# Performance work log

Measured on AMD Instinct MI355X. Metric: run time of the kernel, lower is better.

## Reference

```python
import jax, jax.numpy as jnp
import numpy as np

D = 2048      # in_features (model dim)
H = 1408      # d_intermediate (hidden per expert)
E = 16        # n_routed_experts
T = 16384     # flattened tokens
K = 4         # top_k experts per token


def setup_inputs() -> dict:
    key = jax.random.key(0)
    k1, k2, k3, k4, k5 = jax.random.split(key, 5)
    x = jax.random.normal(k1, (T, D), dtype=jnp.float32)
    weights = jax.random.uniform(k2, (T, K), dtype=jnp.float32)
    indices = jax.random.randint(k3, (T, K), 0, E)
    # Stacked GatedMLP params (bias=False as in mamba's GatedMLP):
    # fc1: [2H, D] per expert, fc2: [D, H] per expert
    W1 = jax.random.normal(k4, (E, 2 * H, D), dtype=jnp.float32) * (D ** -0.5)
    W2 = jax.random.normal(k5, (E, D, H), dtype=jnp.float32) * (H ** -0.5)
    return {"x": x, "weights": weights, "indices": indices, "W1": W1, "W2": W2}


def reference(x, weights, indices, W1, W2):
    # y[t] = sum_i ( GatedMLP_i(x[t]) * sum_k weights[t,k] * [indices[t,k]==i] )
    n_experts = W1.shape[0]
    y = jnp.zeros_like(x)
    for i in range(n_experts):  # small fixed expert loop
        # combined routing weight of expert i per token (handles duplicate hits like += in torch)
        cw = jnp.sum(weights * (indices == i), axis=-1)      # [T]
        h = x @ W1[i].T                                      # [T, 2H]
        u, g = jnp.split(h, 2, axis=-1)                      # chunk(2, dim=-1): (y, gate)
        out = (u * jax.nn.silu(g)) @ W2[i].T                 # [T, D]
        y = y + out * cw[:, None]
    return y
```

## Files before the change

### kernel.cpp

```cpp
#include <hip/hip_runtime.h>

#define D_ 2048
#define H_ 1408
#define E_ 16
#define T_ 16384
#define K_ 4
#define TK_ 65536
#define BM_ 256
#define BK_ 64
#define MAXT_ 272

typedef __attribute__((ext_vector_type(8))) short bf16x8;
typedef __attribute__((ext_vector_type(4))) float f32x4;
typedef __attribute__((ext_vector_type(4))) unsigned short u16x4;
typedef __attribute__((ext_vector_type(8))) unsigned short u16x8;

#define M_COUNTS 0
#define M_OFF    16
#define M_CUR    33
#define M_NT     49
#define M_TE     64
#define M_TR     (64 + MAXT_)
#define M_TN     (64 + 2*MAXT_)

#define XB_OFF   0ULL
#define W1B_OFF  67108864ULL
#define W2B_OFF  (W1B_OFF + 188743680ULL)
#define ACT_OFF  (W2B_OFF + 94371840ULL)
#define PERM_OFF (ACT_OFF + 184549376ULL)
#define WGT_OFF  (PERM_OFF + 262144ULL)
#define META_B   (WGT_OFF + 262144ULL)
#define INV_OFF  (META_B + 65536ULL)
#define YP_OFF   (INV_OFF + 262144ULL)
#define WS_NEED  (YP_OFF + 268435456ULL)

#define SBAR()  __builtin_amdgcn_s_barrier()
#define SCHED() __builtin_amdgcn_sched_barrier(0)
#define LGK0()  asm volatile("s_waitcnt lgkmcnt(0)" ::: "memory")
#define LGK2()  asm volatile("s_waitcnt lgkmcnt(2)" ::: "memory")
#define LGK4()  asm volatile("s_waitcnt lgkmcnt(4)" ::: "memory")
#define LGK6()  asm volatile("s_waitcnt lgkmcnt(6)" ::: "memory")
#define VM6()   asm volatile("s_waitcnt vmcnt(6)" ::: "memory")
#define PRIO1() __builtin_amdgcn_s_setprio(1)
#define PRIO0() __builtin_amdgcn_s_setprio(0)

static __device__ __forceinline__ unsigned short f2bf(float f) {
  unsigned u = __builtin_bit_cast(unsigned, f);
  u += 0x7fffu + ((u >> 16) & 1u);
  return (unsigned short)(u >> 16);
}
static __device__ __forceinline__ float bf2f(unsigned short s) {
  return __builtin_bit_cast(float, (unsigned)s << 16);
}

static __device__ __forceinline__ void gload16(const void* g, unsigned ldsOff) {
  __builtin_amdgcn_global_load_lds(
      (const __attribute__((address_space(1))) unsigned int*)(unsigned long long)g,
      (__attribute__((address_space(3))) unsigned int*)(unsigned long long)ldsOff,
      16, 0, 0);
}

__global__ void cvt3_kernel(const float* __restrict__ x, const float* __restrict__ W1,
                            const float* __restrict__ W2, unsigned short* __restrict__ xb,
                            unsigned short* __restrict__ w1b, unsigned short* __restrict__ w2b) {
  const long long base = ((long long)blockIdx.x * blockDim.x + threadIdx.x) * 4;
  const long long stride = (long long)gridDim.x * blockDim.x * 4;
  for (long long i = base; i < (long long)T_ * D_; i += stride) {
    float4 v = *reinterpret_cast<const float4*>(x + i);
    u16x4 o = { f2bf(v.x), f2bf(v.y), f2bf(v.z), f2bf(v.w) };
    *reinterpret_cast<u16x4*>(xb + i) = o;
  }
  for (long long i = base; i < (long long)E_ * 2 * H_ * D_; i += stride) {
    float4 v = *reinterpret_cast<const float4*>(W1 + i);
    u16x4 o = { f2bf(v.x), f2bf(v.y), f2bf(v.z), f2bf(v.w) };
    *reinterpret_cast<u16x4*>(w1b + i) = o;
  }
  for (long long i = base; i < (long long)E_ * D_ * H_; i += stride) {
    float4 v = *reinterpret_cast<const float4*>(W2 + i);
    u16x4 o = { f2bf(v.x), f2bf(v.y), f2bf(v.z), f2bf(v.w) };
    *reinterpret_cast<u16x4*>(w2b + i) = o;
  }
}

__global__ void route_count(const int* __restrict__ idx, int* __restrict__ meta) {
  int i = blockIdx.x * 256 + threadIdx.x;
  if (i < TK_) atomicAdd(&meta[M_COUNTS + idx[i]], 1);
}

__global__ void scan_build(int* __restrict__ meta) {
  if (threadIdx.x != 0 || blockIdx.x != 0) return;
  int off = 0;
  for (int e = 0; e < E_; ++e) {
    meta[M_OFF + e] = off;
    meta[M_CUR + e] = off;
    off += meta[M_COUNTS + e];
  }
  meta[M_OFF + E_] = off;
  int nt = 0;
  for (int e = 0; e < E_; ++e) {
    int c = meta[M_COUNTS + e], b = meta[M_OFF + e];
    for (int r = 0; r < c; r += BM_) {
      meta[M_TE + nt] = e;
      meta[M_TR + nt] = b + r;
      meta[M_TN + nt] = (c - r < BM_) ? (c - r) : BM_;
      ++nt;
    }
  }
  meta[M_NT] = nt;
}

__global__ void route_fill(const int* __restrict__ idx, const float* __restrict__ wts,
                           int* __restrict__ meta, int* __restrict__ perm,
                           float* __restrict__ wgt, int* __restrict__ inv) {
  int i = blockIdx.x * 256 + threadIdx.x;
  if (i >= TK_) return;
  int e = idx[i];
  int pos = atomicAdd(&meta[M_CUR + e], 1);
  perm[pos] = i >> 2;
  wgt[pos] = wts[i];
  inv[i] = pos;
}

__global__ __launch_bounds__(512, 2) void gemm1_kernel(
    const char* __restrict__ xb, const char* __restrict__ w1b,
    const int* __restrict__ perm, const int* __restrict__ meta,
    unsigned short* __restrict__ act) {
  __shared__ char lds[131072];
  int bid = (int)blockIdx.x;
  bid = (bid & 7) * (int)(gridDim.x >> 3) + (bid >> 3);
  const int tb = bid / 11;
  const int cb = bid - tb * 11;
  if (tb >= meta[M_NT]) return;
  const int e = meta[M_TE + tb];
  const int row0 = meta[M_TR + tb];
  const int nrows = meta[M_TN + tb];
  const int tid = threadIdx.x, lane = tid & 63, wid = tid >> 6;
  const int wr = wid >> 2, wc = wid & 3;
  const unsigned ldsBase = (unsigned)(unsigned long long)&lds[0];
  constexpr int NT = D_ / BK_;

  const char* aSrc[4];
  const char* bSrc[4];
  {
    const int r8 = tid >> 3;
    const unsigned colb0 = (unsigned)(tid & 7) * 16u;
#pragma unroll
    for (int i = 0; i < 4; ++i) {
      const int r = r8 + i * 64;
      const unsigned colb = colb0 ^ ((unsigned)(r & 7) << 4);
      const int rc = (r < nrows) ? r : 0;
      aSrc[i] = xb + (size_t)perm[row0 + rc] * 4096 + colb;
      const int w1row = (i < 2) ? (cb * 128 + r) : (H_ + cb * 128 + (r - 128));
      bSrc[i] = w1b + (size_t)e * (2 * H_) * 4096ULL + (size_t)w1row * 4096 + colb;
    }
  }

  const int l15 = lane & 15, hi = lane >> 4;
  const unsigned swz = (unsigned)(l15 & 7) << 4;
  unsigned aOff[8], bOffU[2], bOffG[2];
#pragma unroll
  for (int m = 0; m < 8; ++m) {
    const int row = wr * 128 + m * 16 + l15;
    aOff[m] = (unsigned)(row * 128) + (((unsigned)hi * 16u) ^ swz);
  }
#pragma unroll
  for (int n = 0; n < 2; ++n) {
    const int ru = wc * 32 + n * 16 + l15;
    bOffU[n] = 65536u + (unsigned)(ru * 128) + (((unsigned)hi * 16u) ^ swz);
    const int rg = ru + 128;
    bOffG[n] = 65536u + (unsigned)(rg * 128) + (((unsigned)hi * 16u) ^ swz);
  }

  f32x4 aU[8][2], aG[8][2];
#pragma unroll
  for (int m = 0; m < 8; ++m)
#pragma unroll
    for (int n = 0; n < 2; ++n) {
      aU[m][n] = (f32x4){0.f, 0.f, 0.f, 0.f};
      aG[m][n] = (f32x4){0.f, 0.f, 0.f, 0.f};
    }

  auto STAGE_A = [&](int t, int h) {
    const int tt = (t < NT) ? t : (NT - 1);
    const size_t kb = (size_t)tt * 128;
    const unsigned dst = ldsBase + (unsigned)(t & 1) * 32768u + (unsigned)h * 16384u + (unsigned)tid * 16u;
    gload16(aSrc[h * 2 + 0] + kb, dst);
    gload16(aSrc[h * 2 + 1] + kb, dst + 8192u);
  };
  auto STAGE_B = [&](int t, int h) {
    const int tt = (t < NT) ? t : (NT - 1);
    const size_t kb = (size_t)tt * 128;
    const unsigned dst = ldsBase + 65536u + (unsigned)(t & 1) * 32768u + (unsigned)h * 16384u + (unsigned)tid * 16u;
    gload16(bSrc[h * 2 + 0] + kb, dst);
    gload16(bSrc[h * 2 + 1] + kb, dst + 8192u);
  };

  STAGE_B(0, 0); STAGE_B(0, 1); STAGE_A(0, 0); STAGE_A(0, 1);
  STAGE_B(1, 0); STAGE_B(1, 1); STAGE_A(1, 0);
  VM6(); SCHED(); SBAR();

  for (int t = 0; t < NT; ++t) {
    const char* base = lds + (unsigned)(t & 1) * 32768u;
    bf16x8 aLo[4][2], aHi[4][2], bu[2][2], bg[2][2];

#pragma unroll
    for (int ks = 0; ks < 2; ++ks) {
#pragma unroll
      for (int m = 0; m < 4; ++m)
        aLo[m][ks] = *reinterpret_cast<const bf16x8*>(base + (aOff[m] ^ (unsigned)(ks << 6)));
#pragma unroll
      for (int n = 0; n < 2; ++n)
        bu[n][ks] = *reinterpret_cast<const bf16x8*>(base + (bOffU[n] ^ (unsigned)(ks << 6)));
    }
    STAGE_A(t + 1, 1);
    SCHED(); SBAR(); LGK6(); SCHED();
    PRIO1();
#pragma unroll
    for (int m = 0; m < 4; ++m)
#pragma unroll
      for (int n = 0; n < 2; ++n)
        aU[m][n] = __builtin_amdgcn_mfma_f32_16x16x32_bf16(aLo[m][0], bu[n][0], aU[m][n], 0, 0, 0);
    LGK0(); SCHED();
#pragma unroll
    for (int m = 0; m < 4; ++m)
#pragma unroll
      for (int n = 0; n < 2; ++n)
        aU[m][n] = __builtin_amdgcn_mfma_f32_16x16x32_bf16(aLo[m][1], bu[n][1], aU[m][n], 0, 0, 0);
    PRIO0(); SCHED(); SBAR();

#pragma unroll
    for (int ks = 0; ks < 2; ++ks)
#pragma unroll
      for (int n = 0; n < 2; ++n)
        bg[n][ks] = *reinterpret_cast<const bf16x8*>(base + (bOffG[n] ^ (unsigned)(ks << 6)));
    STAGE_B(t + 2, 0);
    SCHED(); SBAR(); LGK2(); SCHED();
    PRIO1();
#pragma unroll
    for (int m = 0; m < 4; ++m)
#pragma unroll
      for (int n = 0; n < 2; ++n)
        aG[m][n] = __builtin_amdgcn_mfma_f32_16x16x32_bf16(aLo[m][0], bg[n][0], aG[m][n], 0, 0, 0);
    LGK0(); SCHED();
#pragma unroll
    for (int m = 0; m < 4; ++m)
#pragma unroll
      for (int n = 0; n < 2; ++n)
        aG[m][n] = __builtin_amdgcn_mfma_f32_16x16x32_bf16(aLo[m][1], bg[n][1], aG[m][n], 0, 0, 0);
    PRIO0(); SCHED(); SBAR();

#pragma unroll
    for (int ks = 0; ks < 2; ++ks)
#pragma unroll
      for (int m = 0; m < 4; ++m)
        aHi[m][ks] = *reinterpret_cast<const bf16x8*>(base + (aOff[4 + m] ^ (unsigned)(ks << 6)));
    STAGE_B(t + 2, 1);
    SCHED(); SBAR(); LGK4(); SCHED();
    PRIO1();
#pragma unroll
    for (int m = 0; m < 4; ++m)
#pragma unroll
      for (int n = 0; n < 2; ++n)
        aU[4 + m][n] = __builtin_amdgcn_mfma_f32_16x16x32_bf16(aHi[m][0], bu[n][0], aU[4 + m][n], 0, 0, 0);
    LGK0(); SCHED();
#pragma unroll
    for (int m = 0; m < 4; ++m)
#pragma unroll
      for (int n = 0; n < 2; ++n)
        aU[4 + m][n] = __builtin_amdgcn_mfma_f32_16x16x32_bf16(aHi[m][1], bu[n][1], aU[4 + m][n], 0, 0, 0);
    PRIO0(); SCHED(); SBAR();

    STAGE_A(t + 2, 0);
    VM6(); SCHED(); SBAR();
    PRIO1();
#pragma unroll
    for (int ks = 0; ks < 2; ++ks)
#pragma unroll
      for (int m = 0; m < 4; ++m)
#pragma unroll
        for (int n = 0; n < 2; ++n)
          aG[4 + m][n] = __builtin_amdgcn_mfma_f32_16x16x32_bf16(aHi[m][ks], bg[n][ks], aG[4 + m][n], 0, 0, 0);
    PRIO0(); SCHED(); SBAR();
  }

#pragma unroll
  for (int m = 0; m < 8; ++m)
#pragma unroll
    for (int j = 0; j < 4; ++j) {
      const int r = wr * 128 + m * 16 + hi * 4 + j;
      if (r < nrows) {
        const size_t rowBase = (size_t)(row0 + r) * H_ + (size_t)cb * 128 + (size_t)wc * 32;
#pragma unroll
        for (int n = 0; n < 2; ++n) {
          const float u = aU[m][n][j];
          const float g = aG[m][n][j];
          act[rowBase + n * 16 + l15] = f2bf(u * (g / (1.0f + __expf(-g))));
        }
      }
    }
}

template <int ATOMIC>
__global__ __launch_bounds__(512, 2) void gemm2_kernel(
    const char* __restrict__ actb, const char* __restrict__ w2b,
    const int* __restrict__ perm, const float* __restrict__ wgt,
    const int* __restrict__ meta, unsigned short* __restrict__ yp,
    float* __restrict__ y) {
  __shared__ char lds[131072];
  int bid = (int)blockIdx.x;
  bid = (bid & 7) * (int)(gridDim.x >> 3) + (bid >> 3);
  const int tb = bid >> 3;
  const int cb = bid & 7;
  if (tb >= meta[M_NT]) return;
  const int e = meta[M_TE + tb];
  const int row0 = meta[M_TR + tb];
  const int nrows = meta[M_TN + tb];
  const int tid = threadIdx.x, lane = tid & 63, wid = tid >> 6;
  const int wr = wid >> 2, wc = wid & 3;
  const unsigned ldsBase = (unsigned)(unsigned long long)&lds[0];
  constexpr int NT = H_ / BK_;

  const char* aSrc[4];
  const char* bSrc[4];
  {
    const int r8 = tid >> 3;
    const unsigned colb0 = (unsigned)(tid & 7) * 16u;
#pragma unroll
    for (int i = 0; i < 4; ++i) {
      const int r = r8 + i * 64;
      const unsigned colb = colb0 ^ ((unsigned)(r & 7) << 4);
      const int rc = (r < nrows) ? r : 0;
      aSrc[i] = actb + (size_t)(row0 + rc) * (H_ * 2) + colb;
      const int brow = cb * 256 + r;
      bSrc[i] = w2b + (size_t)e * D_ * (H_ * 2) + (size_t)brow * (H_ * 2) + colb;
    }
  }

  const int l15 = lane & 15, hi = lane >> 4;
  const unsigned swz = (unsigned)(l15 & 7) << 4;
  unsigned aOff[8], bOff[4];
#pragma unroll
  for (int m = 0; m < 8; ++m) {
    const int row = wr * 128 + m * 16 + l15;
    aOff[m] = (unsigned)(row * 128) + (((unsigned)hi * 16u) ^ swz);
  }
#pragma unroll
  for (int n = 0; n < 4; ++n) {
    const int rb = wc * 64 + n * 16 + l15;
    bOff[n] = 65536u + (unsigned)(rb * 128) + (((unsigned)hi * 16u) ^ swz);
  }

  f32x4 acc[8][4];
#pragma unroll
  for (int m = 0; m < 8; ++m)
#pragma unroll
    for (int n = 0; n < 4; ++n) acc[m][n] = (f32x4){0.f, 0.f, 0.f, 0.f};

  auto STAGE_A = [&](int t, int h) {
    const int tt = (t < NT) ? t : (NT - 1);
    const size_t kb = (size_t)tt * 128;
    const unsigned dst = ldsBase + (unsigned)(t & 1) * 32768u + (unsigned)h * 16384u + (unsigned)tid * 16u;
    gload16(aSrc[h * 2 + 0] + kb, dst);
    gload16(aSrc[h * 2 + 1] + kb, dst + 8192u);
  };
  auto STAGE_B = [&](int t, int h) {
    const int tt = (t < NT) ? t : (NT - 1);
    const size_t kb = (size_t)tt * 128;
    const unsigned dst = ldsBase + 65536u + (unsigned)(t & 1) * 32768u + (unsigned)h * 16384u + (unsigned)tid * 16u;
    gload16(bSrc[h * 2 + 0] + kb, dst);
    gload16(bSrc[h * 2 + 1] + kb, dst + 8192u);
  };

  STAGE_B(0, 0); STAGE_B(0, 1); STAGE_A(0, 0); STAGE_A(0, 1);
  STAGE_B(1, 0); STAGE_B(1, 1); STAGE_A(1, 0);
  VM6(); SCHED(); SBAR();

  for (int t = 0; t < NT; ++t) {
    const char* base = lds + (unsigned)(t & 1) * 32768u;
    bf16x8 aLo[4][2], aHi[4][2], b[4][2];

#pragma unroll
    for (int ks = 0; ks < 2; ++ks) {
#pragma unroll
      for (int m = 0; m < 4; ++m)
        aLo[m][ks] = *reinterpret_cast<const bf16x8*>(base + (aOff[m] ^ (unsigned)(ks << 6)));
#pragma unroll
      for (int n = 0; n < 2; ++n)
        b[n][ks] = *reinterpret_cast<const bf16x8*>(base + (bOff[n] ^ (unsigned)(ks << 6)));
    }
    STAGE_A(t + 1, 1);
    SCHED(); SBAR(); LGK6(); SCHED();
    PRIO1();
#pragma unroll
    for (int m = 0; m < 4; ++m)
#pragma unroll
      for (int n = 0; n < 2; ++n)
        acc[m][n] = __builtin_amdgcn_mfma_f32_16x16x32_bf16(aLo[m][0], b[n][0], acc[m][n], 0, 0, 0);
    LGK0(); SCHED();
#pragma unroll
    for (int m = 0; m < 4; ++m)
#pragma unroll
      for (int n = 0; n < 2; ++n)
        acc[m][n] = __builtin_amdgcn_mfma_f32_16x16x32_bf16(aLo[m][1], b[n][1], acc[m][n], 0, 0, 0);
    PRIO0(); SCHED(); SBAR();

#pragma unroll
    for (int ks = 0; ks < 2; ++ks)
#pragma unroll
      for (int n = 2; n < 4; ++n)
        b[n][ks] = *reinterpret_cast<const bf16x8*>(base + (bOff[n] ^ (unsigned)(ks << 6)));
    STAGE_B(t + 2, 0);
    SCHED(); SBAR(); LGK2(); SCHED();
    PRIO1();
#pragma unroll
    for (int m = 0; m < 4; ++m)
#pragma unroll
      for (int n = 2; n < 4; ++n)
        acc[m][n] = __builtin_amdgcn_mfma_f32_16x16x32_bf16(aLo[m][0], b[n][0], acc[m][n], 0, 0, 0);
    LGK0(); SCHED();
#pragma unroll
    for (int m = 0; m < 4; ++m)
#pragma unroll
      for (int n = 2; n < 4; ++n)
        acc[m][n] = __builtin_amdgcn_mfma_f32_16x16x32_bf16(aLo[m][1], b[n][1], acc[m][n], 0, 0, 0);
    PRIO0(); SCHED(); SBAR();

#pragma unroll
    for (int ks = 0; ks < 2; ++ks)
#pragma unroll
      for (int m = 0; m < 4; ++m)
        aHi[m][ks] = *reinterpret_cast<const bf16x8*>(base + (aOff[4 + m] ^ (unsigned)(ks << 6)));
    STAGE_B(t + 2, 1);
    SCHED(); SBAR(); LGK4(); SCHED();
    PRIO1();
#pragma unroll
    for (int m = 0; m < 4; ++m)
#pragma unroll
      for (int n = 0; n < 2; ++n)
        acc[4 + m][n] = __builtin_amdgcn_mfma_f32_16x16x32_bf16(aHi[m][0], b[n][0], acc[4 + m][n], 0, 0, 0);
    LGK0(); SCHED();
#pragma unroll
    for (int m = 0; m < 4; ++m)
#pragma unroll
      for (int n = 0; n < 2; ++n)
        acc[4 + m][n] = __builtin_amdgcn_mfma_f32_16x16x32_bf16(aHi[m][1], b[n][1], acc[4 + m][n], 0, 0, 0);
    PRIO0(); SCHED(); SBAR();

    STAGE_A(t + 2, 0);
    VM6(); SCHED(); SBAR();
    PRIO1();
#pragma unroll
    for (int ks = 0; ks < 2; ++ks)
#pragma unroll
      for (int m = 0; m < 4; ++m)
#pragma unroll
        for (int n = 2; n < 4; ++n)
          acc[4 + m][n] = __builtin_amdgcn_mfma_f32_16x16x32_bf16(aHi[m][ks], b[n][ks], acc[4 + m][n], 0, 0, 0);
    PRIO0(); SCHED(); SBAR();
  }

#pragma unroll
  for (int m = 0; m < 8; ++m)
#pragma unroll
    for (int j = 0; j < 4; ++j) {
      const int r = wr * 128 + m * 16 + hi * 4 + j;
      if (r < nrows) {
        const float w = wgt[row0 + r];
        if (ATOMIC) {
          const int token = perm[row0 + r];
          float* yrow = y + (size_t)token * D_ + (size_t)cb * 256 + (size_t)wc * 64;
#pragma unroll
          for (int n = 0; n < 4; ++n)
            unsafeAtomicAdd(&yrow[n * 16 + l15], acc[m][n][j] * w);
        } else {
          unsigned short* prow = yp + (size_t)(row0 + r) * D_ + (size_t)cb * 256 + (size_t)wc * 64;
#pragma unroll
          for (int n = 0; n < 4; ++n)
            prow[n * 16 + l15] = f2bf(acc[m][n][j] * w);
        }
      }
    }
}

__global__ __launch_bounds__(256) void gather_kernel(
    const unsigned short* __restrict__ yp, const int* __restrict__ inv,
    float* __restrict__ y) {
  const int t = blockIdx.x;
  const int d0 = threadIdx.x * 8;
  int pos[4];
#pragma unroll
  for (int k = 0; k < 4; ++k) pos[k] = inv[t * 4 + k];
  float s[8];
#pragma unroll
  for (int i = 0; i < 8; ++i) s[i] = 0.f;
#pragma unroll
  for (int k = 0; k < 4; ++k) {
    u16x8 v = *reinterpret_cast<const u16x8*>(yp + (size_t)pos[k] * D_ + d0);
#pragma unroll
    for (int i = 0; i < 8; ++i) s[i] += bf2f(v[i]);
  }
  float4 lo = {s[0], s[1], s[2], s[3]}, hi4 = {s[4], s[5], s[6], s[7]};
  *reinterpret_cast<float4*>(y + (size_t)t * D_ + d0) = lo;
  *reinterpret_cast<float4*>(y + (size_t)t * D_ + d0 + 4) = hi4;
}

extern "C" void kernel_launch(void* const* d_in, const int* in_sizes, int n_in,
                              void* d_out, int out_size, void* d_ws, size_t ws_size,
                              hipStream_t stream) {
  const float* x   = (const float*)d_in[0];
  const float* wts = (const float*)d_in[1];
  const int*   idx = (const int*)d_in[2];
  const float* W1  = (const float*)d_in[3];
  const float* W2  = (const float*)d_in[4];
  float* y = (float*)d_out;
  char* ws = (char*)d_ws;

  unsigned short* xb  = (unsigned short*)(ws + XB_OFF);
  unsigned short* w1b = (unsigned short*)(ws + W1B_OFF);
  unsigned short* w2b = (unsigned short*)(ws + W2B_OFF);
  unsigned short* act = (unsigned short*)(ws + ACT_OFF);
  int*   perm = (int*)(ws + PERM_OFF);
  float* wgt  = (float*)(ws + WGT_OFF);
  int*   meta = (int*)(ws + META_B);
  int*   inv  = (int*)(ws + INV_OFF);
  unsigned short* yp = (unsigned short*)(ws + YP_OFF);

  const bool useYp = (ws_size >= (size_t)WS_NEED);

  hipMemsetAsync(meta, 0, 64 * sizeof(int), stream);
  if (!useYp) hipMemsetAsync(d_out, 0, (size_t)out_size * sizeof(float), stream);

  cvt3_kernel<<<4096, 256, 0, stream>>>(x, W1, W2, xb, w1b, w2b);

  route_count<<<TK_ / 256, 256, 0, stream>>>(idx, meta);
  scan_build<<<1, 64, 0, stream>>>(meta);
  route_fill<<<TK_ / 256, 256, 0, stream>>>(idx, wts, meta, perm, wgt, inv);

  gemm1_kernel<<<MAXT_ * (H_ / 128), 512, 0, stream>>>(
      (const char*)xb, (const char*)w1b, perm, meta, act);

  if (useYp) {
    gemm2_kernel<0><<<MAXT_ * (D_ / 256), 512, 0, stream>>>(
        (const char*)act, (const char*)w2b, perm, wgt, meta, yp, y);
    gather_kernel<<<T_, 256, 0, stream>>>(yp, inv, y);
  } else {
    gemm2_kernel<1><<<MAXT_ * (D_ / 256), 512, 0, stream>>>(
        (const char*)act, (const char*)w2b, perm, wgt, meta, yp, y);
  }
}
```

Before: 1.722 ms.

## Use hybrid bf16 partial buffer plus atomic tail to fit smaller workspace

Reorganizes the workspace so the partial-output buffer aliases the dead xb/w1b region. This lets the non-atomic bf16 partial path run without the large extra workspace. Rows below a fixed position threshold write bf16 partials that are gathered later, and the remaining rows use atomic adds into a zeroed output. The gather kernel now does a read-modify-write on y, and the output must always be memset. This avoids falling back to all-atomic accumulation when workspace is limited, at the cost of an extra memset and the y read in the gather.

```diff
diff --git a/kernel.cpp b/kernel.cpp
--- a/kernel.cpp
+++ b/kernel.cpp
@@ -9,6 +9,7 @@
 #define BM_ 256
 #define BK_ 64
 #define MAXT_ 272
+#define P1_ 61440
 
 typedef __attribute__((ext_vector_type(8))) short bf16x8;
 typedef __attribute__((ext_vector_type(4))) float f32x4;
@@ -23,16 +24,15 @@
 #define M_TR     (64 + MAXT_)
 #define M_TN     (64 + 2*MAXT_)
 
-#define XB_OFF   0ULL
-#define W1B_OFF  67108864ULL
-#define W2B_OFF  (W1B_OFF + 188743680ULL)
-#define ACT_OFF  (W2B_OFF + 94371840ULL)
-#define PERM_OFF (ACT_OFF + 184549376ULL)
+#define META_B   0ULL
+#define PERM_OFF 65536ULL
 #define WGT_OFF  (PERM_OFF + 262144ULL)
-#define META_B   (WGT_OFF + 262144ULL)
-#define INV_OFF  (META_B + 65536ULL)
-#define YP_OFF   (INV_OFF + 262144ULL)
-#define WS_NEED  (YP_OFF + 268435456ULL)
+#define INV_OFF  (WGT_OFF + 262144ULL)
+#define ACT_OFF  1048576ULL
+#define W2B_OFF  (ACT_OFF + 184549376ULL)
+#define XB_OFF   (W2B_OFF + 92274688ULL)
+#define W1B_OFF  (XB_OFF + 67108864ULL)
+#define YP_OFF   XB_OFF
 
 #define SBAR()  __builtin_amdgcn_s_barrier()
 #define SCHED() __builtin_amdgcn_sched_barrier(0)
@@ -300,7 +300,6 @@
     }
 }
 
-template <int ATOMIC>
 __global__ __launch_bounds__(512, 2) void gemm2_kernel(
     const char* __restrict__ actb, const char* __restrict__ w2b,
     const int* __restrict__ perm, const float* __restrict__ wgt,
@@ -465,18 +464,19 @@
     for (int j = 0; j < 4; ++j) {
       const int r = wr * 128 + m * 16 + hi * 4 + j;
       if (r < nrows) {
-        const float w = wgt[row0 + r];
-        if (ATOMIC) {
-          const int token = perm[row0 + r];
+        const int posr = row0 + r;
+        const float w = wgt[posr];
+        if (posr < P1_) {
+          unsigned short* prow = yp + (size_t)posr * D_ + (size_t)cb * 256 + (size_t)wc * 64;
+#pragma unroll
+          for (int n = 0; n < 4; ++n)
+            prow[n * 16 + l15] = f2bf(acc[m][n][j] * w);
+        } else {
+          const int token = perm[posr];
           float* yrow = y + (size_t)token * D_ + (size_t)cb * 256 + (size_t)wc * 64;
 #pragma unroll
           for (int n = 0; n < 4; ++n)
             unsafeAtomicAdd(&yrow[n * 16 + l15], acc[m][n][j] * w);
-        } else {
-          unsigned short* prow = yp + (size_t)(row0 + r) * D_ + (size_t)cb * 256 + (size_t)wc * 64;
-#pragma unroll
-          for (int n = 0; n < 4; ++n)
-            prow[n * 16 + l15] = f2bf(acc[m][n][j] * w);
         }
       }
     }
@@ -495,13 +495,19 @@
   for (int i = 0; i < 8; ++i) s[i] = 0.f;
 #pragma unroll
   for (int k = 0; k < 4; ++k) {
-    u16x8 v = *reinterpret_cast<const u16x8*>(yp + (size_t)pos[k] * D_ + d0);
-#pragma unroll
-    for (int i = 0; i < 8; ++i) s[i] += bf2f(v[i]);
-  }
-  float4 lo = {s[0], s[1], s[2], s[3]}, hi4 = {s[4], s[5], s[6], s[7]};
-  *reinterpret_cast<float4*>(y + (size_t)t * D_ + d0) = lo;
-  *reinterpret_cast<float4*>(y + (size_t)t * D_ + d0 + 4) = hi4;
+    if (pos[k] < P1_) {
+      u16x8 v = *reinterpret_cast<const u16x8*>(yp + (size_t)pos[k] * D_ + d0);
+#pragma unroll
+      for (int i = 0; i < 8; ++i) s[i] += bf2f(v[i]);
+    }
+  }
+  float* yrow = y + (size_t)t * D_ + d0;
+  float4 lo = *reinterpret_cast<const float4*>(yrow);
+  float4 hi4 = *reinterpret_cast<const float4*>(yrow + 4);
+  lo.x += s[0]; lo.y += s[1]; lo.z += s[2]; lo.w += s[3];
+  hi4.x += s[4]; hi4.y += s[5]; hi4.z += s[6]; hi4.w += s[7];
+  *reinterpret_cast<float4*>(yrow) = lo;
+  *reinterpret_cast<float4*>(yrow + 4) = hi4;
 }
 
 extern "C" void kernel_launch(void* const* d_in, const int* in_sizes, int n_in,
@@ -515,20 +521,18 @@
   float* y = (float*)d_out;
   char* ws = (char*)d_ws;
 
+  int*   meta = (int*)(ws + META_B);
+  int*   perm = (int*)(ws + PERM_OFF);
+  float* wgt  = (float*)(ws + WGT_OFF);
+  int*   inv  = (int*)(ws + INV_OFF);
+  unsigned short* act = (unsigned short*)(ws + ACT_OFF);
+  unsigned short* w2b = (unsigned short*)(ws + W2B_OFF);
   unsigned short* xb  = (unsigned short*)(ws + XB_OFF);
   unsigned short* w1b = (unsigned short*)(ws + W1B_OFF);
-  unsigned short* w2b = (unsigned short*)(ws + W2B_OFF);
-  unsigned short* act = (unsigned short*)(ws + ACT_OFF);
-  int*   perm = (int*)(ws + PERM_OFF);
-  float* wgt  = (float*)(ws + WGT_OFF);
-  int*   meta = (int*)(ws + META_B);
-  int*   inv  = (int*)(ws + INV_OFF);
-  unsigned short* yp = (unsigned short*)(ws + YP_OFF);
-
-  const bool useYp = (ws_size >= (size_t)WS_NEED);
+  unsigned short* yp  = (unsigned short*)(ws + YP_OFF);
 
   hipMemsetAsync(meta, 0, 64 * sizeof(int), stream);
-  if (!useYp) hipMemsetAsync(d_out, 0, (size_t)out_size * sizeof(float), stream);
+  hipMemsetAsync(d_out, 0, (size_t)out_size * sizeof(float), stream);
 
   cvt3_kernel<<<4096, 256, 0, stream>>>(x, W1, W2, xb, w1b, w2b);
 
@@ -539,12 +543,8 @@
   gemm1_kernel<<<MAXT_ * (H_ / 128), 512, 0, stream>>>(
       (const char*)xb, (const char*)w1b, perm, meta, act);
 
-  if (useYp) {
-    gemm2_kernel<0><<<MAXT_ * (D_ / 256), 512, 0, stream>>>(
-        (const char*)act, (const char*)w2b, perm, wgt, meta, yp, y);
-    gather_kernel<<<T_, 256, 0, stream>>>(yp, inv, y);
-  } else {
-    gemm2_kernel<1><<<MAXT_ * (D_ / 256), 512, 0, stream>>>(
-        (const char*)act, (const char*)w2b, perm, wgt, meta, yp, y);
-  }
-}
+  gemm2_kernel<<<MAXT_ * (D_ / 256), 512, 0, stream>>>(
+      (const char*)act, (const char*)w2b, perm, wgt, meta, yp, y);
+
+  gather_kernel<<<T_, 256, 0, stream>>>(yp, inv, y);
+}
```

New measurement: 1.800 ms. 1.05x slower.

## Drop workgroup barriers in GEMM main loops and scatter output via atomics

Applied to the files above, without the earlier changes.

Removes several s_barrier calls inside the main loops of both GEMM kernels, keeping only the per-wave LDS waitcnt and the one barrier after the vmcnt wait. Drops the bf16 per-slot partial buffer and its gather kernel. The second GEMM now always accumulates weighted results straight into the zeroed fp32 output with atomic adds. The aim is to cut cross-wave stalls, one kernel launch and the partial-buffer traffic, in exchange for float atomic contention and a possible LDS reuse race.

```diff
diff --git a/kernel.cpp b/kernel.cpp
--- a/kernel.cpp
+++ b/kernel.cpp
@@ -13,7 +13,6 @@
 typedef __attribute__((ext_vector_type(8))) short bf16x8;
 typedef __attribute__((ext_vector_type(4))) float f32x4;
 typedef __attribute__((ext_vector_type(4))) unsigned short u16x4;
-typedef __attribute__((ext_vector_type(8))) unsigned short u16x8;
 
 #define M_COUNTS 0
 #define M_OFF    16
@@ -30,9 +29,6 @@
 #define PERM_OFF (ACT_OFF + 184549376ULL)
 #define WGT_OFF  (PERM_OFF + 262144ULL)
 #define META_B   (WGT_OFF + 262144ULL)
-#define INV_OFF  (META_B + 65536ULL)
-#define YP_OFF   (INV_OFF + 262144ULL)
-#define WS_NEED  (YP_OFF + 268435456ULL)
 
 #define SBAR()  __builtin_amdgcn_s_barrier()
 #define SCHED() __builtin_amdgcn_sched_barrier(0)
@@ -49,9 +45,6 @@
   u += 0x7fffu + ((u >> 16) & 1u);
   return (unsigned short)(u >> 16);
 }
-static __device__ __forceinline__ float bf2f(unsigned short s) {
-  return __builtin_bit_cast(float, (unsigned)s << 16);
-}
 
 static __device__ __forceinline__ void gload16(const void* g, unsigned ldsOff) {
   __builtin_amdgcn_global_load_lds(
@@ -111,14 +104,13 @@
 
 __global__ void route_fill(const int* __restrict__ idx, const float* __restrict__ wts,
                            int* __restrict__ meta, int* __restrict__ perm,
-                           float* __restrict__ wgt, int* __restrict__ inv) {
+                           float* __restrict__ wgt) {
   int i = blockIdx.x * 256 + threadIdx.x;
   if (i >= TK_) return;
   int e = idx[i];
   int pos = atomicAdd(&meta[M_CUR + e], 1);
   perm[pos] = i >> 2;
   wgt[pos] = wts[i];
-  inv[i] = pos;
 }
 
 __global__ __launch_bounds__(512, 2) void gemm1_kernel(
@@ -213,7 +205,7 @@
         bu[n][ks] = *reinterpret_cast<const bf16x8*>(base + (bOffU[n] ^ (unsigned)(ks << 6)));
     }
     STAGE_A(t + 1, 1);
-    SCHED(); SBAR(); LGK6(); SCHED();
+    LGK6(); SCHED();
     PRIO1();
 #pragma unroll
     for (int m = 0; m < 4; ++m)
@@ -234,7 +226,7 @@
       for (int n = 0; n < 2; ++n)
         bg[n][ks] = *reinterpret_cast<const bf16x8*>(base + (bOffG[n] ^ (unsigned)(ks << 6)));
     STAGE_B(t + 2, 0);
-    SCHED(); SBAR(); LGK2(); SCHED();
+    LGK2(); SCHED();
     PRIO1();
 #pragma unroll
     for (int m = 0; m < 4; ++m)
@@ -255,7 +247,7 @@
       for (int m = 0; m < 4; ++m)
         aHi[m][ks] = *reinterpret_cast<const bf16x8*>(base + (aOff[4 + m] ^ (unsigned)(ks << 6)));
     STAGE_B(t + 2, 1);
-    SCHED(); SBAR(); LGK4(); SCHED();
+    LGK4(); SCHED();
     PRIO1();
 #pragma unroll
     for (int m = 0; m < 4; ++m)
@@ -280,7 +272,7 @@
 #pragma unroll
         for (int n = 0; n < 2; ++n)
           aG[4 + m][n] = __builtin_amdgcn_mfma_f32_16x16x32_bf16(aHi[m][ks], bg[n][ks], aG[4 + m][n], 0, 0, 0);
-    PRIO0(); SCHED(); SBAR();
+    PRIO0(); SCHED();
   }
 
 #pragma unroll
@@ -300,12 +292,10 @@
     }
 }
 
-template <int ATOMIC>
 __global__ __launch_bounds__(512, 2) void gemm2_kernel(
     const char* __restrict__ actb, const char* __restrict__ w2b,
     const int* __restrict__ perm, const float* __restrict__ wgt,
-    const int* __restrict__ meta, unsigned short* __restrict__ yp,
-    float* __restrict__ y) {
+    const int* __restrict__ meta, float* __restrict__ y) {
   __shared__ char lds[131072];
   int bid = (int)blockIdx.x;
   bid = (bid & 7) * (int)(gridDim.x >> 3) + (bid >> 3);
@@ -389,7 +379,7 @@
         b[n][ks] = *reinterpret_cast<const bf16x8*>(base + (bOff[n] ^ (unsigned)(ks << 6)));
     }
     STAGE_A(t + 1, 1);
-    SCHED(); SBAR(); LGK6(); SCHED();
+    LGK6(); SCHED();
     PRIO1();
 #pragma unroll
     for (int m = 0; m < 4; ++m)
@@ -410,7 +400,7 @@
       for (int n = 2; n < 4; ++n)
         b[n][ks] = *reinterpret_cast<const bf16x8*>(base + (bOff[n] ^ (unsigned)(ks << 6)));
     STAGE_B(t + 2, 0);
-    SCHED(); SBAR(); LGK2(); SCHED();
+    LGK2(); SCHED();
     PRIO1();
 #pragma unroll
     for (int m = 0; m < 4; ++m)
@@ -431,7 +421,7 @@
       for (int m = 0; m < 4; ++m)
         aHi[m][ks] = *reinterpret_cast<const bf16x8*>(base + (aOff[4 + m] ^ (unsigned)(ks << 6)));
     STAGE_B(t + 2, 1);
-    SCHED(); SBAR(); LGK4(); SCHED();
+    LGK4(); SCHED();
     PRIO1();
 #pragma unroll
     for (int m = 0; m < 4; ++m)
@@ -456,7 +446,7 @@
 #pragma unroll
         for (int n = 2; n < 4; ++n)
           acc[4 + m][n] = __builtin_amdgcn_mfma_f32_16x16x32_bf16(aHi[m][ks], b[n][ks], acc[4 + m][n], 0, 0, 0);
-    PRIO0(); SCHED(); SBAR();
+    PRIO0(); SCHED();
   }
 
 #pragma unroll
@@ -466,42 +456,13 @@
       const int r = wr * 128 + m * 16 + hi * 4 + j;
       if (r < nrows) {
         const float w = wgt[row0 + r];
-        if (ATOMIC) {
-          const int token = perm[row0 + r];
-          float* yrow = y + (size_t)token * D_ + (size_t)cb * 256 + (size_t)wc * 64;
-#pragma unroll
-          for (int n = 0; n < 4; ++n)
-            unsafeAtomicAdd(&yrow[n * 16 + l15], acc[m][n][j] * w);
-        } else {
-          unsigned short* prow = yp + (size_t)(row0 + r) * D_ + (size_t)cb * 256 + (size_t)wc * 64;
-#pragma unroll
-          for (int n = 0; n < 4; ++n)
-            prow[n * 16 + l15] = f2bf(acc[m][n][j] * w);
-        }
+        const int token = perm[row0 + r];
+        float* yrow = y + (size_t)token * D_ + (size_t)cb * 256 + (size_t)wc * 64;
+#pragma unroll
+        for (int n = 0; n < 4; ++n)
+          unsafeAtomicAdd(&yrow[n * 16 + l15], acc[m][n][j] * w);
       }
     }
-}
-
-__global__ __launch_bounds__(256) void gather_kernel(
-    const unsigned short* __restrict__ yp, const int* __restrict__ inv,
-    float* __restrict__ y) {
-  const int t = blockIdx.x;
-  const int d0 = threadIdx.x * 8;
-  int pos[4];
-#pragma unroll
-  for (int k = 0; k < 4; ++k) pos[k] = inv[t * 4 + k];
-  float s[8];
-#pragma unroll
-  for (int i = 0; i < 8; ++i) s[i] = 0.f;
-#pragma unroll
-  for (int k = 0; k < 4; ++k) {
-    u16x8 v = *reinterpret_cast<const u16x8*>(yp + (size_t)pos[k] * D_ + d0);
-#pragma unroll
-    for (int i = 0; i < 8; ++i) s[i] += bf2f(v[i]);
-  }
-  float4 lo = {s[0], s[1], s[2], s[3]}, hi4 = {s[4], s[5], s[6], s[7]};
-  *reinterpret_cast<float4*>(y + (size_t)t * D_ + d0) = lo;
-  *reinterpret_cast<float4*>(y + (size_t)t * D_ + d0 + 4) = hi4;
 }
 
 extern "C" void kernel_launch(void* const* d_in, const int* in_sizes, int n_in,
@@ -522,29 +483,19 @@
   int*   perm = (int*)(ws + PERM_OFF);
   float* wgt  = (float*)(ws + WGT_OFF);
   int*   meta = (int*)(ws + META_B);
-  int*   inv  = (int*)(ws + INV_OFF);
-  unsigned short* yp = (unsigned short*)(ws + YP_OFF);
-
-  const bool useYp = (ws_size >= (size_t)WS_NEED);
 
   hipMemsetAsync(meta, 0, 64 * sizeof(int), stream);
-  if (!useYp) hipMemsetAsync(d_out, 0, (size_t)out_size * sizeof(float), stream);
+  hipMemsetAsync(d_out, 0, (size_t)out_size * sizeof(float), stream);
 
   cvt3_kernel<<<4096, 256, 0, stream>>>(x, W1, W2, xb, w1b, w2b);
 
   route_count<<<TK_ / 256, 256, 0, stream>>>(idx, meta);
   scan_build<<<1, 64, 0, stream>>>(meta);
-  route_fill<<<TK_ / 256, 256, 0, stream>>>(idx, wts, meta, perm, wgt, inv);
+  route_fill<<<TK_ / 256, 256, 0, stream>>>(idx, wts, meta, perm, wgt);
 
   gemm1_kernel<<<MAXT_ * (H_ / 128), 512, 0, stream>>>(
       (const char*)xb, (const char*)w1b, perm, meta, act);
 
-  if (useYp) {
-    gemm2_kernel<0><<<MAXT_ * (D_ / 256), 512, 0, stream>>>(
-        (const char*)act, (const char*)w2b, perm, wgt, meta, yp, y);
-    gather_kernel<<<T_, 256, 0, stream>>>(yp, inv, y);
-  } else {
-    gemm2_kernel<1><<<MAXT_ * (D_ / 256), 512, 0, stream>>>(
-        (const char*)act, (const char*)w2b, perm, wgt, meta, yp, y);
-  }
-}
+  gemm2_kernel<<<MAXT_ * (D_ / 256), 512, 0, stream>>>(
+      (const char*)act, (const char*)w2b, perm, wgt, meta, y);
+}
```

Measured after the change: 1.832 ms. +6.4%, slower.
